# Performance work log

Hardware: AMD Instinct MI355X
Metric: run time of the kernel (lower is better)

## Reference

```python
import jax, jax.numpy as jnp
import numpy as np

BLOCK = 128  # fp8 block-quant block size (128, 128)


def dequant_block_fp8_weight(w, scale_inv):
    """w: [O, I] fp8-valued weights (stored as f32); scale_inv: [O//128, I//128].
    Dequant = per-(128,128)-block multiply by scale."""
    O, I = w.shape
    wb = w.reshape(O // BLOCK, BLOCK, I // BLOCK, BLOCK)
    wb = wb * scale_inv[:, None, :, None]
    return wb.reshape(O, I)


def setup_inputs() -> dict:
    key = jax.random.key(0)
    ks = jax.random.split(key, 7)
    H, F, T = 5120, 1536, 8192  # hidden, moe_intermediate, tokens
    x = jax.random.normal(ks[0], (T, H), dtype=jnp.float32)
    w_gate = jax.random.normal(ks[1], (F, H), dtype=jnp.float32)
    s_gate = jax.random.uniform(ks[2], (F // BLOCK, H // BLOCK), dtype=jnp.float32) * 0.01 + 1e-4
    w_up = jax.random.normal(ks[3], (F, H), dtype=jnp.float32)
    s_up = jax.random.uniform(ks[4], (F // BLOCK, H // BLOCK), dtype=jnp.float32) * 0.01 + 1e-4
    w_down = jax.random.normal(ks[5], (H, F), dtype=jnp.float32)
    s_down = jax.random.uniform(ks[6], (H // BLOCK, F // BLOCK), dtype=jnp.float32) * 0.01 + 1e-4
    return {"x": x, "w_gate": w_gate, "s_gate": s_gate, "w_up": w_up,
            "s_up": s_up, "w_down": w_down, "s_down": s_down}


def reference(x, w_gate, s_gate, w_up, s_up, w_down, s_down):
    # down_proj(silu(gate_proj(x)) * up_proj(x)), each Linear dequantizing
    # block-scaled fp8 weights first (bias=False everywhere).
    wg = dequant_block_fp8_weight(w_gate, s_gate).astype(x.dtype)
    wu = dequant_block_fp8_weight(w_up, s_up).astype(x.dtype)
    wd = dequant_block_fp8_weight(w_down, s_down).astype(x.dtype)
    gate = jnp.einsum('th,fh->tf', x, wg)  # [T, F]
    up = jnp.einsum('th,fh->tf', x, wu)    # [T, F]
    h = jax.nn.silu(gate) * up
    out = jnp.einsum('tf,hf->th', h, wd)   # [T, H]
    return out
```

## Files before the change

kernel.cpp:

```cpp
#include <hip/hip_runtime.h>


typedef __bf16 bf16x8 __attribute__((ext_vector_type(8)));
typedef float  f32x4  __attribute__((ext_vector_type(4)));

__device__ __forceinline__ void glds16(const __bf16* g, __bf16* l) {
  __builtin_amdgcn_global_load_lds(
      (const __attribute__((address_space(1))) void*)g,
      (__attribute__((address_space(3))) void*)l, 16, 0, 0);
}

__device__ __forceinline__ void chunk_rk(int c, int& row, int& k) {
  int s = c >> 6;
  int w = (c & 63) << 4;
  int wl = w ^ (((w >> 9) & 1) << 5) ^ (((w >> 7) & 1) << 4);
  row = (s << 4) + (wl >> 6);
  k = (wl & 63) >> 1;
}

#define SYNC(n)                                                        \
  do {                                                                 \
    __builtin_amdgcn_sched_barrier(0);                                 \
    asm volatile("s_waitcnt vmcnt(" #n ")\n\ts_barrier" ::: "memory"); \
    __builtin_amdgcn_sched_barrier(0);                                 \
  } while (0)

__device__ __forceinline__ void cast8(const float* __restrict__ in,
                                      __bf16* __restrict__ out, size_t idx) {
  f32x4 a = *(const f32x4*)(in + idx);
  f32x4 b = *(const f32x4*)(in + idx + 4);
  bf16x8 o;
#pragma unroll
  for (int i = 0; i < 4; ++i) { o[i] = (__bf16)a[i]; o[i + 4] = (__bf16)b[i]; }
  *(bf16x8*)(out + idx) = o;
}

__device__ __forceinline__ void dq_ilv(const float* __restrict__ w,
                                       const float* __restrict__ s,
                                       __bf16* __restrict__ wq, int r, int tid,
                                       int which) {
  unsigned idx = ((unsigned)r * 256u + (unsigned)tid) * 8u;
  unsigned f = idx / 5120u;
  unsigned h = idx - f * 5120u;
  float sc = s[(f >> 7) * 40 + (h >> 7)];
  f32x4 a = *(const f32x4*)(w + idx);
  f32x4 b = *(const f32x4*)(w + idx + 4);
  bf16x8 o;
#pragma unroll
  for (int i = 0; i < 4; ++i) {
    o[i] = (__bf16)(a[i] * sc);
    o[i + 4] = (__bf16)(b[i] * sc);
  }
  *(bf16x8*)(wq + (size_t)(2 * f + which) * 5120 + h) = o;
}

__device__ __forceinline__ void dq_wd(const float* __restrict__ w,
                                      const float* __restrict__ s,
                                      __bf16* __restrict__ o8, int r, int tid) {
  unsigned idx = ((unsigned)r * 256u + (unsigned)tid) * 8u;
  unsigned f = idx / 1536u;
  unsigned h = idx - f * 1536u;
  float sc = s[(f >> 7) * 12 + (h >> 7)];
  f32x4 a = *(const f32x4*)(w + idx);
  f32x4 b = *(const f32x4*)(w + idx + 4);
  bf16x8 o;
#pragma unroll
  for (int i = 0; i < 4; ++i) {
    o[i] = (__bf16)(a[i] * sc);
    o[i + 4] = (__bf16)(b[i] * sc);
  }
  *(bf16x8*)(o8 + idx) = o;
}

__global__ void prep(const float* __restrict__ x, const float* __restrict__ wg,
                     const float* __restrict__ sg, const float* __restrict__ wu,
                     const float* __restrict__ su, const float* __restrict__ wd,
                     const float* __restrict__ sd, __bf16* __restrict__ xb,
                     __bf16* __restrict__ wq, __bf16* __restrict__ wdq) {
  int bid = blockIdx.x;
  int tid = threadIdx.x;
  if (bid < 20480) {
    cast8(x, xb, ((size_t)bid * 256 + tid) * 8);
  } else if (bid < 24320) {
    dq_ilv(wg, sg, wq, bid - 20480, tid, 0);
  } else if (bid < 28160) {
    dq_ilv(wu, su, wq, bid - 24320, tid, 1);
  } else {
    dq_wd(wd, sd, wdq, bid - 28160, tid);
  }
}

template <bool FUSE_SILU, typename OutT>
__global__ __launch_bounds__(512, 2) void gemm_p(
    const __bf16* __restrict__ A, const __bf16* __restrict__ B,
    OutT* __restrict__ C, int M, int N, int K, int ldc, int nbx) {
  __shared__ __bf16 lds[4 * 12288];
  const int tid = threadIdx.x;
  const int lane = tid & 63;
  const int wave = tid >> 6;
  const int lr = lane & 15;

  const int nwg = gridDim.x;
  const int lb = (blockIdx.x & 7) * (nwg >> 3) + (blockIdx.x >> 3);
  const int bx = lb % nbx;
  const int by = lb / nbx;
  const int m0 = by * 128, n0 = bx * 256;

  int laneoff = (lr << 6) | ((lane >> 4) << 4);
  laneoff ^= ((lr & 2) << 3) | ((lr & 8) << 2);
  const int wm4 = wave & 4;
  const int wn4 = (wave & 3) << 2;

  int ra, ka, rb0, kb0, rb1, kb1;
  chunk_rk(tid, ra, ka);
  chunk_rk(tid, rb0, kb0);
  chunk_rk(tid + 512, rb1, kb1);
  const __bf16* Ab = A + (size_t)m0 * K;
  const __bf16* Bb = B + (size_t)n0 * K;
  const unsigned offA = (unsigned)ra * K + (unsigned)ka;
  const unsigned offB0 = (unsigned)rb0 * K + (unsigned)kb0;
  const unsigned offB1 = (unsigned)rb1 * K + (unsigned)kb1;

  f32x4 acc[4][4] = {};

  auto STAGE = [&](int t, int bufi) {
    __bf16* lb_ = lds + bufi * 12288;
    const unsigned ko = (unsigned)t << 5;
    glds16(Ab + (offA + ko), lb_ + (tid << 3));
    glds16(Bb + (offB0 + ko), lb_ + 4096 + (tid << 3));
    glds16(Bb + (offB1 + ko), lb_ + 4096 + ((tid + 512) << 3));
  };
  auto COMPUTE = [&](int bufi) {
    const char* base = (const char*)lds + bufi * 24576;
    bf16x8 af[4], bg[4];
#pragma unroll
    for (int i = 0; i < 4; ++i)
      af[i] = *(const bf16x8*)(base + ((wm4 + i) << 10) + laneoff);
#pragma unroll
    for (int j = 0; j < 4; ++j)
      bg[j] = *(const bf16x8*)(base + 8192 + ((wn4 + j) << 10) + laneoff);
    __builtin_amdgcn_s_setprio(1);
#pragma unroll
    for (int j = 0; j < 4; ++j)
#pragma unroll
      for (int i = 0; i < 4; ++i)
        acc[i][j] = __builtin_amdgcn_mfma_f32_16x16x32_bf16(af[i], bg[j],
                                                            acc[i][j], 0, 0, 0);
    __builtin_amdgcn_s_setprio(0);
  };

  const int NT = K >> 5;
  STAGE(0, 0);
  STAGE(1, 1);
  STAGE(2, 2);
  SYNC(6);
  int cur = 0;
  for (int t = 0; t < NT - 3; ++t) {
    STAGE(t + 3, (cur + 3) & 3);
    COMPUTE(cur);
    SYNC(6);
    cur = (cur + 1) & 3;
  }
  COMPUTE(cur); SYNC(3); cur = (cur + 1) & 3;
  COMPUTE(cur); SYNC(0); cur = (cur + 1) & 3;
  COMPUTE(cur);

  const int colb = n0 + (wn4 << 4) + lr;
  const int rowb = m0 + (wm4 << 4) + ((lane >> 4) << 2);
#pragma unroll
  for (int i = 0; i < 4; ++i)
#pragma unroll
    for (int j = 0; j < 4; ++j)
#pragma unroll
      for (int r = 0; r < 4; ++r) {
        if constexpr (FUSE_SILU) {
          float v = acc[i][j][r];
          float p = __shfl_xor(v, 1, 64);
          float g = (lane & 1) ? p : v;
          float u = (lane & 1) ? v : p;
          float hv = (g / (1.0f + __expf(-g))) * u;
          if ((lane & 1) == 0)
            C[(size_t)(rowb + i * 16 + r) * ldc + ((colb + j * 16) >> 1)] =
                (OutT)hv;
        } else {
          C[(size_t)(rowb + i * 16 + r) * ldc + (colb + j * 16)] =
              (OutT)acc[i][j][r];
        }
      }
}

extern "C" void kernel_launch(void* const* d_in, const int* in_sizes, int n_in,
                              void* d_out, int out_size, void* d_ws,
                              size_t ws_size, hipStream_t stream) {
  const int Hd = 5120, Fd = 1536, Td = 8192;
  const float* x = (const float*)d_in[0];
  const float* wg = (const float*)d_in[1];
  const float* sg = (const float*)d_in[2];
  const float* wu = (const float*)d_in[3];
  const float* su = (const float*)d_in[4];
  const float* wd = (const float*)d_in[5];
  const float* sd = (const float*)d_in[6];
  float* out = (float*)d_out;

  __bf16* ws = (__bf16*)d_ws;
  const size_t xsz = (size_t)Td * Hd;
  __bf16* xb = ws;
  __bf16* wq = xb + xsz;
  __bf16* wdq = wq + (size_t)2 * Fd * Hd;
  __bf16* hbuf = wdq + (size_t)Hd * Fd;

  prep<<<32000, 256, 0, stream>>>(x, wg, sg, wu, su, wd, sd, xb, wq, wdq);

  gemm_p<true, __bf16><<<768, 512, 0, stream>>>(xb, wq, hbuf, Td, 2 * Fd, Hd,
                                                Fd, 12);

  gemm_p<false, float><<<1280, 512, 0, stream>>>(hbuf, wdq, out, Td, Hd, Fd,
                                                 Hd, 20);
}
```

Baseline: 792.7 us.

## Restructure GEMM mainloop into split-phase triple-buffered pipeline with higher occupancy

Replaces the 4-stage LDS ring with a 3-stage ring and splits each K-step into two half-phases that interleave LDS reads, global-to-LDS prefetch issue and MFMA groups, separated by workgroup barriers. Cutting LDS from 96KB to 72KB per block and raising launch bounds to 4 waves-per-EU target is meant to allow more resident blocks and finer overlap of loads with MFMA. The cost is a shallower prefetch depth, extra barriers per iteration, and register pressure from the higher launch-bounds target, which may cause spills.

```diff
diff --git a/kernel.cpp b/kernel.cpp
--- a/kernel.cpp
+++ b/kernel.cpp
@@ -18,7 +18,14 @@
   k = (wl & 63) >> 1;
 }
 
-#define SYNC(n)                                                        \
+#define BAR()                                      \
+  do {                                             \
+    __builtin_amdgcn_sched_barrier(0);             \
+    asm volatile("s_barrier" ::: "memory");        \
+    __builtin_amdgcn_sched_barrier(0);             \
+  } while (0)
+
+#define VMBAR(n)                                                       \
   do {                                                                 \
     __builtin_amdgcn_sched_barrier(0);                                 \
     asm volatile("s_waitcnt vmcnt(" #n ")\n\ts_barrier" ::: "memory"); \
@@ -91,10 +98,10 @@
 }
 
 template <bool FUSE_SILU, typename OutT>
-__global__ __launch_bounds__(512, 2) void gemm_p(
+__global__ __launch_bounds__(512, 4) void gemm_p(
     const __bf16* __restrict__ A, const __bf16* __restrict__ B,
     OutT* __restrict__ C, int M, int N, int K, int ldc, int nbx) {
-  __shared__ __bf16 lds[4 * 12288];
+  __shared__ __bf16 lds[3 * 12288];
   const int tid = threadIdx.x;
   const int lane = tid & 63;
   const int wave = tid >> 6;
@@ -122,48 +129,81 @@
   const unsigned offB1 = (unsigned)rb1 * K + (unsigned)kb1;
 
   f32x4 acc[4][4] = {};
-
-  auto STAGE = [&](int t, int bufi) {
+  bf16x8 af[4], bg[4];
+
+  auto STAGE_AB0 = [&](int t, int bufi) {
     __bf16* lb_ = lds + bufi * 12288;
     const unsigned ko = (unsigned)t << 5;
     glds16(Ab + (offA + ko), lb_ + (tid << 3));
     glds16(Bb + (offB0 + ko), lb_ + 4096 + (tid << 3));
+  };
+  auto STAGE_B1 = [&](int t, int bufi) {
+    __bf16* lb_ = lds + bufi * 12288;
+    const unsigned ko = (unsigned)t << 5;
     glds16(Bb + (offB1 + ko), lb_ + 4096 + ((tid + 512) << 3));
   };
-  auto COMPUTE = [&](int bufi) {
+  auto RD_A = [&](int bufi) {
     const char* base = (const char*)lds + bufi * 24576;
-    bf16x8 af[4], bg[4];
 #pragma unroll
     for (int i = 0; i < 4; ++i)
       af[i] = *(const bf16x8*)(base + ((wm4 + i) << 10) + laneoff);
-#pragma unroll
-    for (int j = 0; j < 4; ++j)
-      bg[j] = *(const bf16x8*)(base + 8192 + ((wn4 + j) << 10) + laneoff);
+  };
+  auto RD_B = [&](int bufi, int j0) {
+    const char* base = (const char*)lds + bufi * 24576 + 8192;
+#pragma unroll
+    for (int j = 0; j < 2; ++j)
+      bg[j0 + j] = *(const bf16x8*)(base + ((wn4 + j0 + j) << 10) + laneoff);
+  };
+  auto MFMA2 = [&](int j0) {
     __builtin_amdgcn_s_setprio(1);
 #pragma unroll
-    for (int j = 0; j < 4; ++j)
+    for (int j = 0; j < 2; ++j)
 #pragma unroll
       for (int i = 0; i < 4; ++i)
-        acc[i][j] = __builtin_amdgcn_mfma_f32_16x16x32_bf16(af[i], bg[j],
-                                                            acc[i][j], 0, 0, 0);
+        acc[i][j0 + j] = __builtin_amdgcn_mfma_f32_16x16x32_bf16(
+            af[i], bg[j0 + j], acc[i][j0 + j], 0, 0, 0);
     __builtin_amdgcn_s_setprio(0);
   };
 
   const int NT = K >> 5;
-  STAGE(0, 0);
-  STAGE(1, 1);
-  STAGE(2, 2);
-  SYNC(6);
-  int cur = 0;
-  for (int t = 0; t < NT - 3; ++t) {
-    STAGE(t + 3, (cur + 3) & 3);
-    COMPUTE(cur);
-    SYNC(6);
-    cur = (cur + 1) & 3;
-  }
-  COMPUTE(cur); SYNC(3); cur = (cur + 1) & 3;
-  COMPUTE(cur); SYNC(0); cur = (cur + 1) & 3;
-  COMPUTE(cur);
+
+  STAGE_AB0(0, 0);
+  STAGE_B1(0, 0);
+  STAGE_AB0(1, 1);
+  STAGE_B1(1, 1);
+  VMBAR(3);
+
+  int cur = 0, stg = 2;
+  for (int t = 0; t < NT - 2; ++t) {
+    RD_A(cur);
+    RD_B(cur, 0);
+    STAGE_AB0(t + 2, stg);
+    BAR();
+    MFMA2(0);
+    BAR();
+    RD_B(cur, 2);
+    STAGE_B1(t + 2, stg);
+    BAR();
+    MFMA2(2);
+    VMBAR(3);
+    cur = (cur == 2) ? 0 : cur + 1;
+    stg = (stg == 2) ? 0 : stg + 1;
+  }
+  RD_A(cur);
+  RD_B(cur, 0);
+  BAR();
+  MFMA2(0);
+  BAR();
+  RD_B(cur, 2);
+  BAR();
+  MFMA2(2);
+  VMBAR(0);
+  cur = (cur == 2) ? 0 : cur + 1;
+  RD_A(cur);
+  RD_B(cur, 0);
+  MFMA2(0);
+  RD_B(cur, 2);
+  MFMA2(2);
 
   const int colb = n0 + (wn4 << 4) + lr;
   const int rowb = m0 + (wm4 << 4) + ((lane >> 4) << 2);
```

New measurement: 740.5 us. 1.07x faster.

## Enlarge GEMM tile to 256x256 with split-phase LDS reads and barriers

Applied to the files above, without the earlier changes.

The block tile grows from 128x256 to 256x256, so each wave now holds 8x4 accumulators, and each k-step is split into two half-phases, each with its own LDS fragment read, barrier and MFMA batch. The goal is more operand reuse per LDS byte and less global traffic per FLOP, with loads interleaved between the MFMA halves. LDS use grows to 128KB per block and register pressure rises, which puts the 2-blocks-per-CU launch bound and occupancy at risk. The grid sizes are halved to match, and the extra barriers add synchronisation cost.

```diff
diff --git a/kernel.cpp b/kernel.cpp
--- a/kernel.cpp
+++ b/kernel.cpp
@@ -18,7 +18,20 @@
   k = (wl & 63) >> 1;
 }
 
-#define SYNC(n)                                                        \
+#define BAR()                               \
+  do {                                      \
+    __builtin_amdgcn_sched_barrier(0);      \
+    asm volatile("s_barrier" ::: "memory"); \
+    __builtin_amdgcn_sched_barrier(0);      \
+  } while (0)
+
+#define LGKM0()                                        \
+  do {                                                 \
+    asm volatile("s_waitcnt lgkmcnt(0)" ::: "memory"); \
+    __builtin_amdgcn_sched_barrier(0);                 \
+  } while (0)
+
+#define VMBAR(n)                                                       \
   do {                                                                 \
     __builtin_amdgcn_sched_barrier(0);                                 \
     asm volatile("s_waitcnt vmcnt(" #n ")\n\ts_barrier" ::: "memory"); \
@@ -90,11 +103,69 @@
   }
 }
 
+
+#define STAGE_A(t_, es_)                     \
+  do {                                       \
+    __bf16* lp = lds + (es_) * 16384;        \
+    const unsigned ko = (unsigned)(t_) << 5; \
+    glds16(Ab + (off0 + ko), lp + d0);       \
+    glds16(Ab + (off1 + ko), lp + d1);       \
+  } while (0)
+
+#define STAGE_B(t_, es_)                     \
+  do {                                       \
+    __bf16* lp = lds + (es_) * 16384 + 8192; \
+    const unsigned ko = (unsigned)(t_) << 5; \
+    glds16(Bb + (off0 + ko), lp + d0);       \
+    glds16(Bb + (off1 + ko), lp + d1);       \
+  } while (0)
+
+#define RD_AF(e_, h_)                                                       \
+  do {                                                                      \
+    const char* b_ = (const char*)lds + (e_) * 32768;                       \
+    _Pragma("unroll") for (int i = 0; i < 4; ++i) af[i] =                   \
+        *(const bf16x8*)(b_ + ((a_sub + (h_) * 4 + i) << 10) + laneoff);    \
+  } while (0)
+
+#define RD_BG(e_)                                                 \
+  do {                                                            \
+    const char* b_ = (const char*)lds + (e_) * 32768 + 16384;     \
+    _Pragma("unroll") for (int j = 0; j < 4; ++j) bg[j] =         \
+        *(const bf16x8*)(b_ + ((b_sub + j) << 10) + laneoff);     \
+  } while (0)
+
+#define MFMA16(h_)                                                          \
+  do {                                                                      \
+    __builtin_amdgcn_s_setprio(1);                                          \
+    _Pragma("unroll") for (int j = 0; j < 4; ++j)                           \
+        _Pragma("unroll") for (int i = 0; i < 4; ++i) acc[(h_) * 4 + i][j] = \
+            __builtin_amdgcn_mfma_f32_16x16x32_bf16(                        \
+                af[i], bg[j], acc[(h_) * 4 + i][j], 0, 0, 0);               \
+    __builtin_amdgcn_s_setprio(0);                                          \
+  } while (0)
+
+#define KSTEP(e_, SA, SB, TRAIL) \
+  do {                           \
+    RD_AF(e_, 0);                \
+    RD_BG(e_);                   \
+    SA;                          \
+    BAR();                       \
+    LGKM0();                     \
+    MFMA16(0);                   \
+    BAR();                       \
+    RD_AF(e_, 1);                \
+    SB;                          \
+    BAR();                       \
+    LGKM0();                     \
+    MFMA16(1);                   \
+    TRAIL;                       \
+  } while (0)
+
 template <bool FUSE_SILU, typename OutT>
 __global__ __launch_bounds__(512, 2) void gemm_p(
     const __bf16* __restrict__ A, const __bf16* __restrict__ B,
     OutT* __restrict__ C, int M, int N, int K, int ldc, int nbx) {
-  __shared__ __bf16 lds[4 * 12288];
+  __shared__ __bf16 lds[4 * 16384];
   const int tid = threadIdx.x;
   const int lane = tid & 63;
   const int wave = tid >> 6;
@@ -104,71 +175,49 @@
   const int lb = (blockIdx.x & 7) * (nwg >> 3) + (blockIdx.x >> 3);
   const int bx = lb % nbx;
   const int by = lb / nbx;
-  const int m0 = by * 128, n0 = bx * 256;
+  const int m0 = by * 256, n0 = bx * 256;
 
   int laneoff = (lr << 6) | ((lane >> 4) << 4);
   laneoff ^= ((lr & 2) << 3) | ((lr & 8) << 2);
-  const int wm4 = wave & 4;
-  const int wn4 = (wave & 3) << 2;
-
-  int ra, ka, rb0, kb0, rb1, kb1;
-  chunk_rk(tid, ra, ka);
-  chunk_rk(tid, rb0, kb0);
-  chunk_rk(tid + 512, rb1, kb1);
+  const int wrow = wave >> 2;
+  const int wcol = wave & 3;
+  const int a_sub = wrow << 3;
+  const int b_sub = wcol << 2;
+
+  int r0, k0, r1, k1;
+  chunk_rk(tid, r0, k0);
+  chunk_rk(tid + 512, r1, k1);
   const __bf16* Ab = A + (size_t)m0 * K;
   const __bf16* Bb = B + (size_t)n0 * K;
-  const unsigned offA = (unsigned)ra * K + (unsigned)ka;
-  const unsigned offB0 = (unsigned)rb0 * K + (unsigned)kb0;
-  const unsigned offB1 = (unsigned)rb1 * K + (unsigned)kb1;
-
-  f32x4 acc[4][4] = {};
-
-  auto STAGE = [&](int t, int bufi) {
-    __bf16* lb_ = lds + bufi * 12288;
-    const unsigned ko = (unsigned)t << 5;
-    glds16(Ab + (offA + ko), lb_ + (tid << 3));
-    glds16(Bb + (offB0 + ko), lb_ + 4096 + (tid << 3));
-    glds16(Bb + (offB1 + ko), lb_ + 4096 + ((tid + 512) << 3));
-  };
-  auto COMPUTE = [&](int bufi) {
-    const char* base = (const char*)lds + bufi * 24576;
-    bf16x8 af[4], bg[4];
-#pragma unroll
-    for (int i = 0; i < 4; ++i)
-      af[i] = *(const bf16x8*)(base + ((wm4 + i) << 10) + laneoff);
-#pragma unroll
-    for (int j = 0; j < 4; ++j)
-      bg[j] = *(const bf16x8*)(base + 8192 + ((wn4 + j) << 10) + laneoff);
-    __builtin_amdgcn_s_setprio(1);
-#pragma unroll
-    for (int j = 0; j < 4; ++j)
-#pragma unroll
-      for (int i = 0; i < 4; ++i)
-        acc[i][j] = __builtin_amdgcn_mfma_f32_16x16x32_bf16(af[i], bg[j],
-                                                            acc[i][j], 0, 0, 0);
-    __builtin_amdgcn_s_setprio(0);
-  };
+  const unsigned off0 = (unsigned)r0 * K + (unsigned)k0;
+  const unsigned off1 = (unsigned)r1 * K + (unsigned)k1;
+  const int d0 = tid << 3, d1 = (tid + 512) << 3;
+
+  f32x4 acc[8][4] = {};
+  bf16x8 af[4], bg[4];
 
   const int NT = K >> 5;
-  STAGE(0, 0);
-  STAGE(1, 1);
-  STAGE(2, 2);
-  SYNC(6);
-  int cur = 0;
-  for (int t = 0; t < NT - 3; ++t) {
-    STAGE(t + 3, (cur + 3) & 3);
-    COMPUTE(cur);
-    SYNC(6);
-    cur = (cur + 1) & 3;
-  }
-  COMPUTE(cur); SYNC(3); cur = (cur + 1) & 3;
-  COMPUTE(cur); SYNC(0); cur = (cur + 1) & 3;
-  COMPUTE(cur);
-
-  const int colb = n0 + (wn4 << 4) + lr;
-  const int rowb = m0 + (wm4 << 4) + ((lane >> 4) << 2);
-#pragma unroll
-  for (int i = 0; i < 4; ++i)
+
+  STAGE_A(0, 0); STAGE_B(0, 0);
+  STAGE_A(1, 1); STAGE_B(1, 1);
+  STAGE_A(2, 2); STAGE_B(2, 2);
+  VMBAR(8);
+
+  for (int t = 0; t < NT - 4; t += 4) {
+    KSTEP(0, STAGE_A(t + 3, 3), STAGE_B(t + 3, 3), VMBAR(8));
+    KSTEP(1, STAGE_A(t + 4, 0), STAGE_B(t + 4, 0), VMBAR(8));
+    KSTEP(2, STAGE_A(t + 5, 1), STAGE_B(t + 5, 1), VMBAR(8));
+    KSTEP(3, STAGE_A(t + 6, 2), STAGE_B(t + 6, 2), VMBAR(8));
+  }
+  KSTEP(0, STAGE_A(NT - 1, 3), STAGE_B(NT - 1, 3), VMBAR(8));
+  KSTEP(1, (void)0, (void)0, VMBAR(4));
+  KSTEP(2, (void)0, (void)0, VMBAR(0));
+  KSTEP(3, (void)0, (void)0, (void)0);
+
+  const int colb = n0 + (wcol << 6) + lr;
+  const int rowb = m0 + (wrow << 7) + ((lane >> 4) << 2);
+#pragma unroll
+  for (int i = 0; i < 8; ++i)
 #pragma unroll
     for (int j = 0; j < 4; ++j)
 #pragma unroll
@@ -211,9 +260,9 @@
 
   prep<<<32000, 256, 0, stream>>>(x, wg, sg, wu, su, wd, sd, xb, wq, wdq);
 
-  gemm_p<true, __bf16><<<768, 512, 0, stream>>>(xb, wq, hbuf, Td, 2 * Fd, Hd,
+  gemm_p<true, __bf16><<<384, 512, 0, stream>>>(xb, wq, hbuf, Td, 2 * Fd, Hd,
                                                 Fd, 12);
 
-  gemm_p<false, float><<<1280, 512, 0, stream>>>(hbuf, wdq, out, Td, Hd, Fd,
-                                                 Hd, 20);
-}
+  gemm_p<false, float><<<640, 512, 0, stream>>>(hbuf, wdq, out, Td, Hd, Fd,
+                                                Hd, 20);
+}
```

Measured after the change: 749.1 us. 5.5% less time.

## Halve GEMM workgroup to 4 waves with 32x4 tiles and split-phase pipeline

Applied to the files above, without the earlier changes.

Cuts the GEMM workgroup from 8 to 4 waves, so each wave computes a 128x64 tile (8x4 MFMA accumulators) instead of 64x64. The K loop moves from 4 LDS stages to 3, and each step splits into two half-phases that interleave LDS fragment reads, global-to-LDS staging and MFMA bursts with explicit barriers and lgkmcnt waits. The aim is higher per-wave data reuse and better overlap of loads with compute. The cost is higher register pressure from 128 accumulator floats per thread and more barriers per K step.

```diff
diff --git a/kernel.cpp b/kernel.cpp
--- a/kernel.cpp
+++ b/kernel.cpp
@@ -18,7 +18,20 @@
   k = (wl & 63) >> 1;
 }
 
-#define SYNC(n)                                                        \
+#define BAR()                               \
+  do {                                      \
+    __builtin_amdgcn_sched_barrier(0);      \
+    asm volatile("s_barrier" ::: "memory"); \
+    __builtin_amdgcn_sched_barrier(0);      \
+  } while (0)
+
+#define LGKM0()                                        \
+  do {                                                 \
+    asm volatile("s_waitcnt lgkmcnt(0)" ::: "memory"); \
+    __builtin_amdgcn_sched_barrier(0);                 \
+  } while (0)
+
+#define VMBAR(n)                                                       \
   do {                                                                 \
     __builtin_amdgcn_sched_barrier(0);                                 \
     asm volatile("s_waitcnt vmcnt(" #n ")\n\ts_barrier" ::: "memory"); \
@@ -91,10 +104,10 @@
 }
 
 template <bool FUSE_SILU, typename OutT>
-__global__ __launch_bounds__(512, 2) void gemm_p(
+__global__ __launch_bounds__(256, 2) void gemm_p(
     const __bf16* __restrict__ A, const __bf16* __restrict__ B,
     OutT* __restrict__ C, int M, int N, int K, int ldc, int nbx) {
-  __shared__ __bf16 lds[4 * 12288];
+  __shared__ __bf16 lds[3 * 12288];
   const int tid = threadIdx.x;
   const int lane = tid & 63;
   const int wave = tid >> 6;
@@ -108,67 +121,117 @@
 
   int laneoff = (lr << 6) | ((lane >> 4) << 4);
   laneoff ^= ((lr & 2) << 3) | ((lr & 8) << 2);
-  const int wm4 = wave & 4;
-  const int wn4 = (wave & 3) << 2;
-
-  int ra, ka, rb0, kb0, rb1, kb1;
-  chunk_rk(tid, ra, ka);
-  chunk_rk(tid, rb0, kb0);
-  chunk_rk(tid + 512, rb1, kb1);
+  const int b_sub = wave << 2;
+
+  int rr[4], kk[4];
+  chunk_rk(tid, rr[0], kk[0]);
+  chunk_rk(tid + 256, rr[1], kk[1]);
+  chunk_rk(tid + 512, rr[2], kk[2]);
+  chunk_rk(tid + 768, rr[3], kk[3]);
+  const unsigned o0 = (unsigned)rr[0] * K + (unsigned)kk[0];
+  const unsigned o1 = (unsigned)rr[1] * K + (unsigned)kk[1];
+  const unsigned o2 = (unsigned)rr[2] * K + (unsigned)kk[2];
+  const unsigned o3 = (unsigned)rr[3] * K + (unsigned)kk[3];
+  const int d0 = tid << 3, d1 = (tid + 256) << 3;
+  const int d2 = (tid + 512) << 3, d3 = (tid + 768) << 3;
   const __bf16* Ab = A + (size_t)m0 * K;
   const __bf16* Bb = B + (size_t)n0 * K;
-  const unsigned offA = (unsigned)ra * K + (unsigned)ka;
-  const unsigned offB0 = (unsigned)rb0 * K + (unsigned)kb0;
-  const unsigned offB1 = (unsigned)rb1 * K + (unsigned)kb1;
-
-  f32x4 acc[4][4] = {};
-
-  auto STAGE = [&](int t, int bufi) {
-    __bf16* lb_ = lds + bufi * 12288;
+
+  f32x4 acc[8][4] = {};
+  bf16x8 af[4], bg[4];
+
+  auto STAGE_P0 = [&](int t, int s) {
+    __bf16* sb = lds + s * 12288;
     const unsigned ko = (unsigned)t << 5;
-    glds16(Ab + (offA + ko), lb_ + (tid << 3));
-    glds16(Bb + (offB0 + ko), lb_ + 4096 + (tid << 3));
-    glds16(Bb + (offB1 + ko), lb_ + 4096 + ((tid + 512) << 3));
-  };
-  auto COMPUTE = [&](int bufi) {
-    const char* base = (const char*)lds + bufi * 24576;
-    bf16x8 af[4], bg[4];
+    glds16(Ab + (o0 + ko), sb + d0);
+    glds16(Ab + (o1 + ko), sb + d1);
+    glds16(Bb + (o0 + ko), sb + 4096 + d0);
+    glds16(Bb + (o1 + ko), sb + 4096 + d1);
+  };
+  auto STAGE_P1 = [&](int t, int s) {
+    __bf16* sb = lds + s * 12288;
+    const unsigned ko = (unsigned)t << 5;
+    glds16(Bb + (o2 + ko), sb + 4096 + d2);
+    glds16(Bb + (o3 + ko), sb + 4096 + d3);
+  };
+  auto RD_AF = [&](const char* base, int h) {
 #pragma unroll
     for (int i = 0; i < 4; ++i)
-      af[i] = *(const bf16x8*)(base + ((wm4 + i) << 10) + laneoff);
+      af[i] = *(const bf16x8*)(base + (((h << 2) + i) << 10) + laneoff);
+  };
+  auto RD_BG = [&](const char* base) {
 #pragma unroll
     for (int j = 0; j < 4; ++j)
-      bg[j] = *(const bf16x8*)(base + 8192 + ((wn4 + j) << 10) + laneoff);
+      bg[j] = *(const bf16x8*)(base + 8192 + ((b_sub + j) << 10) + laneoff);
+  };
+  auto MFMA16 = [&](int h) {
     __builtin_amdgcn_s_setprio(1);
 #pragma unroll
     for (int j = 0; j < 4; ++j)
 #pragma unroll
       for (int i = 0; i < 4; ++i)
-        acc[i][j] = __builtin_amdgcn_mfma_f32_16x16x32_bf16(af[i], bg[j],
-                                                            acc[i][j], 0, 0, 0);
+        acc[(h << 2) + i][j] = __builtin_amdgcn_mfma_f32_16x16x32_bf16(
+            af[i], bg[j], acc[(h << 2) + i][j], 0, 0, 0);
     __builtin_amdgcn_s_setprio(0);
   };
 
   const int NT = K >> 5;
-  STAGE(0, 0);
-  STAGE(1, 1);
-  STAGE(2, 2);
-  SYNC(6);
-  int cur = 0;
-  for (int t = 0; t < NT - 3; ++t) {
-    STAGE(t + 3, (cur + 3) & 3);
-    COMPUTE(cur);
-    SYNC(6);
-    cur = (cur + 1) & 3;
-  }
-  COMPUTE(cur); SYNC(3); cur = (cur + 1) & 3;
-  COMPUTE(cur); SYNC(0); cur = (cur + 1) & 3;
-  COMPUTE(cur);
-
-  const int colb = n0 + (wn4 << 4) + lr;
-  const int rowb = m0 + (wm4 << 4) + ((lane >> 4) << 2);
-#pragma unroll
-  for (int i = 0; i < 4; ++i)
+
+  STAGE_P0(0, 0);
+  STAGE_P1(0, 0);
+  STAGE_P0(1, 1);
+  STAGE_P1(1, 1);
+  VMBAR(6);
+
+  int cur = 0, stg = 2;
+  for (int t = 0; t < NT - 2; ++t) {
+    const char* cb = (const char*)lds + cur * 24576;
+    RD_AF(cb, 0);
+    RD_BG(cb);
+    STAGE_P0(t + 2, stg);
+    BAR();
+    LGKM0();
+    MFMA16(0);
+    BAR();
+    RD_AF(cb, 1);
+    STAGE_P1(t + 2, stg);
+    BAR();
+    LGKM0();
+    MFMA16(1);
+    VMBAR(6);
+    cur = (cur == 2) ? 0 : cur + 1;
+    stg = (stg == 2) ? 0 : stg + 1;
+  }
+  {
+    const char* cb = (const char*)lds + cur * 24576;
+    RD_AF(cb, 0);
+    RD_BG(cb);
+    BAR();
+    LGKM0();
+    MFMA16(0);
+    BAR();
+    RD_AF(cb, 1);
+    BAR();
+    LGKM0();
+    MFMA16(1);
+    VMBAR(0);
+    cur = (cur == 2) ? 0 : cur + 1;
+  }
+  {
+    const char* cb = (const char*)lds + cur * 24576;
+    RD_AF(cb, 0);
+    RD_BG(cb);
+    LGKM0();
+    MFMA16(0);
+    RD_AF(cb, 1);
+    LGKM0();
+    MFMA16(1);
+  }
+
+  const int colb = n0 + (wave << 6) + lr;
+  const int rowb = m0 + ((lane >> 4) << 2);
+#pragma unroll
+  for (int i = 0; i < 8; ++i)
 #pragma unroll
     for (int j = 0; j < 4; ++j)
 #pragma unroll
@@ -211,9 +274,9 @@
 
   prep<<<32000, 256, 0, stream>>>(x, wg, sg, wu, su, wd, sd, xb, wq, wdq);
 
-  gemm_p<true, __bf16><<<768, 512, 0, stream>>>(xb, wq, hbuf, Td, 2 * Fd, Hd,
+  gemm_p<true, __bf16><<<768, 256, 0, stream>>>(xb, wq, hbuf, Td, 2 * Fd, Hd,
                                                 Fd, 12);
 
-  gemm_p<false, float><<<1280, 512, 0, stream>>>(hbuf, wdq, out, Td, Hd, Fd,
+  gemm_p<false, float><<<1280, 256, 0, stream>>>(hbuf, wdq, out, Td, Hd, Fd,
                                                  Hd, 20);
 }
```

Result: faster. 732.1 us (-7.7%).
